# Performance work log

Hardware: AMD Instinct MI355X
Metric: run time of the kernel (lower is better)

The kernel has to match this reference:

```python
import jax, jax.numpy as jnp
import numpy as np

B = 1
N_ATOM = 2048
N_TOKEN = 512
C = 128      # c_q (atom single channels)
CZ = 16      # c_p (atom pair channels)
H = 4        # no_heads
CH = 32      # c_hidden per head
NB = 3       # no_blocks
NT = 2       # n_transition
NH = NT * C  # transition hidden width
N_QUERY = 32
N_KEY = 128
INF = 1e9


def _ln(x, eps=1e-5):
    m = jnp.mean(x, axis=-1, keepdims=True)
    v = jnp.var(x, axis=-1, keepdims=True)
    return (x - m) * jax.lax.rsqrt(v + eps)


def _adaln(a, s, gs, ws, bs, wsb):
    # AF3 Alg 26: AdaLN(a, s)
    s_n = _ln(s) * gs                      # LayerNorm(s), scale only
    a_n = _ln(a)                           # LayerNorm(a), no affine
    return jax.nn.sigmoid(s_n @ ws + bs) * a_n + s_n @ wsb


def setup_inputs() -> dict:
    key = jax.random.key(0)
    ks = jax.random.split(key, 32)

    def w(k, shape, s=0.02):
        return s * jax.random.normal(k, shape, jnp.float32)

    d = {}
    d["ql"] = jax.random.normal(ks[0], (B, N_ATOM, C), jnp.float32)
    d["cl"] = jax.random.normal(ks[1], (B, N_ATOM, C), jnp.float32)
    d["plm"] = jax.random.normal(ks[2], (B, N_ATOM, N_ATOM, CZ), jnp.float32)
    tok = jnp.arange(N_ATOM) // (N_ATOM // N_TOKEN)          # ~4 atoms per token
    d["atom_to_token_index"] = jnp.broadcast_to(jax.nn.one_hot(tok, N_TOKEN, dtype=jnp.float32), (B, N_ATOM, N_TOKEN)) + 0.0
    d["token_mask"] = jnp.ones((B, N_TOKEN), jnp.float32)

    # AttentionPairBias params (stacked over NB blocks)
    d["ada1_gs"] = jnp.ones((NB, C), jnp.float32)
    d["ada1_ws"] = w(ks[3], (NB, C, C))
    d["ada1_bs"] = jnp.zeros((NB, C), jnp.float32)
    d["ada1_wsb"] = w(ks[4], (NB, C, C))
    d["wq"] = w(ks[5], (NB, C, H, CH))
    d["bq"] = jnp.zeros((NB, H, CH), jnp.float32)
    d["wk"] = w(ks[6], (NB, C, H, CH))
    d["wv"] = w(ks[7], (NB, C, H, CH))
    d["gz"] = jnp.ones((NB, CZ), jnp.float32)
    d["bz"] = jnp.zeros((NB, CZ), jnp.float32)
    d["wz"] = w(ks[8], (NB, CZ, H))
    d["wg"] = w(ks[9], (NB, C, H, CH))
    d["wo"] = w(ks[10], (NB, H, CH, C))
    d["wog1"] = w(ks[11], (NB, C, C))
    d["bog1"] = -2.0 * jnp.ones((NB, C), jnp.float32)
    # ConditionedTransitionBlock params
    d["ada2_gs"] = jnp.ones((NB, C), jnp.float32)
    d["ada2_ws"] = w(ks[12], (NB, C, C))
    d["ada2_bs"] = jnp.zeros((NB, C), jnp.float32)
    d["ada2_wsb"] = w(ks[13], (NB, C, C))
    d["wt1"] = w(ks[14], (NB, C, NH))
    d["wt2"] = w(ks[15], (NB, C, NH))
    d["wt3"] = w(ks[16], (NB, NH, C))
    d["wog2"] = w(ks[17], (NB, C, C))
    d["bog2"] = -2.0 * jnp.ones((NB, C), jnp.float32)
    return d


def _forward(ql, cl, plm, atom_to_token_index, token_mask,
             ada1_gs, ada1_ws, ada1_bs, ada1_wsb, wq, bq, wk, wv,
             gz, bz, wz, wg, wo, wog1, bog1,
             ada2_gs, ada2_ws, ada2_bs, ada2_wsb, wt1, wt2, wt3, wog2, bog2):
    # --- block-sparse (32x128) additive mask, exactly as in the torch module ---
    offset = N_QUERY // 2 - 0.5
    n_center = N_ATOM // N_QUERY + 1
    centers = offset + jnp.arange(n_center, dtype=jnp.float32) * N_QUERY
    ar = jnp.arange(N_ATOM, dtype=jnp.float32)
    row = (jnp.abs(ar[:, None] - centers[None, :]) < N_QUERY / 2).astype(ql.dtype)
    col = (jnp.abs(ar[:, None] - centers[None, :]) < N_KEY / 2).astype(ql.dtype)
    blm = (row @ col.T - 1.0) * INF                          # [N, N] in {0, -inf}

    atom_mask = jnp.einsum("bli,bi->bl", atom_to_token_index, token_mask)
    mask_bias = (atom_mask - 1.0) * INF                      # [B, N] additive key mask

    inv_sqrt_ch = 1.0 / np.sqrt(CH).astype(np.float32)
    a, s = ql, cl
    for b in range(NB):
        # --- AttentionPairBias (AF3 Alg 24) ---
        a_ln = _adaln(a, s, ada1_gs[b], ada1_ws[b], ada1_bs[b], ada1_wsb[b])
        q = jnp.einsum("bnc,chd->bnhd", a_ln, wq[b]) + bq[b]
        k = jnp.einsum("bnc,chd->bnhd", a_ln, wk[b])
        v = jnp.einsum("bnc,chd->bnhd", a_ln, wv[b])
        z_ln = _ln(plm) * gz[b] + bz[b]
        pb = jnp.einsum("bnmc,ch->bhnm", z_ln, wz[b])        # pair bias [B,H,N,N]
        logits = (jnp.einsum("bnhd,bmhd->bhnm", q, k) * inv_sqrt_ch
                  + pb + blm[None, None] + mask_bias[:, None, None, :])
        attn = jax.nn.softmax(logits, axis=-1)
        o = jnp.einsum("bhnm,bmhd->bnhd", attn, v)
        o = jax.nn.sigmoid(jnp.einsum("bnc,chd->bnhd", a_ln, wg[b])) * o
        att_out = jnp.einsum("bnhd,hdc->bnc", o, wo[b])
        att_out = jax.nn.sigmoid(s @ wog1[b] + bog1[b]) * att_out
        # --- ConditionedTransitionBlock (AF3 Alg 25) ---
        a2 = _adaln(a, s, ada2_gs[b], ada2_ws[b], ada2_bs[b], ada2_wsb[b])
        hidden = jax.nn.silu(a2 @ wt1[b]) * (a2 @ wt2[b])    # SwiGLU
        trans = jax.nn.sigmoid(s @ wog2[b] + bog2[b]) * (hidden @ wt3[b])
        a = att_out + trans                                   # AF3 Alg 23 update
    return a


def reference(ql, cl, plm, atom_to_token_index, token_mask,
              ada1_gs, ada1_ws, ada1_bs, ada1_wsb, wq, bq, wk, wv,
              gz, bz, wz, wg, wo, wog1, bog1,
              ada2_gs, ada2_ws, ada2_bs, ada2_wsb, wt1, wt2, wt3, wog2, bog2):
    return _forward(ql, cl, plm, atom_to_token_index, token_mask,
                    ada1_gs, ada1_ws, ada1_bs, ada1_wsb, wq, bq, wk, wv,
                    gz, bz, wz, wg, wo, wog1, bog1,
                    ada2_gs, ada2_ws, ada2_bs, ada2_wsb, wt1, wt2, wt3, wog2, bog2)
```

## Files before the change

kernel.cpp:

```cpp
#include <hip/hip_runtime.h>
#include <math.h>

#define N_ATOM 2048
#define NTOK   512
#define CC     128
#define CZDIM  16
#define HH     4
#define CHD    32
#define NHID   256
#define NQB    64
#define R1     8
#define PBSTRIDE 1048576

__device__ __forceinline__ float sigm(float x) { return 1.0f / (1.0f + __expf(-x)); }

struct SmemU {
    float lna[R1][CC];
    float sn1[R1][CC];
    float sn2[R1][CC];
    float cls[R1][CC];
    float aln1[R1][CC];
    float a2s[R1][CC];
    float hid[R1][NHID];
    float tmpA[4][R1][CC];
    float tmpB[4][R1][CC];
};

template<int LDX>
__device__ __forceinline__ void mv_acc(const float* Xbase, int c0, int nc,
                                       const float* __restrict__ W, int ldw,
                                       int col2, float2 acc[4]) {
    for (int c = c0; c < c0 + nc; c += 4) {
        float2 w0 = *(const float2*)(W + (size_t)(c + 0) * ldw + col2);
        float2 w1 = *(const float2*)(W + (size_t)(c + 1) * ldw + col2);
        float2 w2 = *(const float2*)(W + (size_t)(c + 2) * ldw + col2);
        float2 w3 = *(const float2*)(W + (size_t)(c + 3) * ldw + col2);
#pragma unroll
        for (int r = 0; r < 4; r++) {
            float4 xv = *(const float4*)(Xbase + r * LDX + c);
            acc[r].x += xv.x * w0.x + xv.y * w1.x + xv.z * w2.x + xv.w * w3.x;
            acc[r].y += xv.x * w0.y + xv.y * w1.y + xv.z * w2.y + xv.w * w3.y;
        }
    }
}

__device__ void adaln_proj_body(
    SmemU& sm, int t, int n0,
    const float* __restrict__ gs1, const float* __restrict__ ws1,
    const float* __restrict__ bs1, const float* __restrict__ wsb1,
    const float* __restrict__ wq, const float* __restrict__ bq,
    const float* __restrict__ wk, const float* __restrict__ wv,
    const float* __restrict__ wg,
    const float* __restrict__ wog1, const float* __restrict__ bog1,
    const float* __restrict__ gs2, const float* __restrict__ ws2,
    const float* __restrict__ bs2, const float* __restrict__ wsb2,
    const float* __restrict__ wt1, const float* __restrict__ wt2,
    const float* __restrict__ wt3,
    const float* __restrict__ wog2, const float* __restrict__ bog2,
    float* __restrict__ q_o, float* __restrict__ k_o, float* __restrict__ v_o,
    float* __restrict__ g_o, float* __restrict__ og1_o, float* __restrict__ trans_o) {
    {
        int r = t >> 6, l = t & 63;
        float s = 0, s2 = 0;
#pragma unroll
        for (int k = 0; k < 2; k++) { float x = sm.lna[r][l + 64 * k]; s += x; s2 += x * x; }
        for (int m = 1; m < 64; m <<= 1) { s += __shfl_xor(s, m); s2 += __shfl_xor(s2, m); }
        float mean = s * (1.0f / 128.0f);
        float rs = rsqrtf(s2 * (1.0f / 128.0f) - mean * mean + 1e-5f);
        float cs = 0, cs2 = 0;
#pragma unroll
        for (int k = 0; k < 2; k++) { float x = sm.cls[r][l + 64 * k]; cs += x; cs2 += x * x; }
        for (int m = 1; m < 64; m <<= 1) { cs += __shfl_xor(cs, m); cs2 += __shfl_xor(cs2, m); }
        float cmean = cs * (1.0f / 128.0f);
        float crs = rsqrtf(cs2 * (1.0f / 128.0f) - cmean * cmean + 1e-5f);
#pragma unroll
        for (int k = 0; k < 2; k++) {
            int c = l + 64 * k;
            sm.lna[r][c] = (sm.lna[r][c] - mean) * rs;
            float cn = (sm.cls[r][c] - cmean) * crs;
            sm.sn1[r][c] = cn * gs1[c];
            sm.sn2[r][c] = cn * gs2[c];
        }
    }
    __syncthreads();

    {
        int rh = (t >> 6) & 1, l = t & 63, col2 = 2 * l;
        {
            int s = t >> 7;
            const float* X = (s < 2) ? &sm.sn1[rh * 4][0] : &sm.sn2[rh * 4][0];
            const float* W = (s == 0) ? ws1 : (s == 1) ? wsb1 : (s == 2) ? ws2 : wsb2;
            float2 acc[4] = {{0,0},{0,0},{0,0},{0,0}};
            mv_acc<CC>(X, 0, CC, W, CC, col2, acc);
#pragma unroll
            for (int r = 0; r < 4; r++)
                *(float2*)&sm.tmpA[s][rh * 4 + r][col2] = acc[r];
        }
        {
            int s2 = t >> 8, ch = (t >> 7) & 1;
            const float* W = s2 ? wog2 : wog1;
            float2 acc[4] = {{0,0},{0,0},{0,0},{0,0}};
            mv_acc<CC>(&sm.cls[rh * 4][0], ch * 64, 64, W, CC, col2, acc);
#pragma unroll
            for (int r = 0; r < 4; r++)
                *(float2*)&sm.tmpB[s2 * 2 + ch][rh * 4 + r][col2] = acc[r];
        }
    }
    __syncthreads();

    float G[2];
    {
        int o = t & 127, g = t >> 7;
#pragma unroll
        for (int r = 0; r < 2; r++) {
            int rr = 2 * g + r;
            float A1 = sm.tmpA[0][rr][o], B1 = sm.tmpA[1][rr][o];
            float A2 = sm.tmpA[2][rr][o], B2 = sm.tmpA[3][rr][o];
            float O1 = sm.tmpB[0][rr][o] + sm.tmpB[1][rr][o];
            float O2 = sm.tmpB[2][rr][o] + sm.tmpB[3][rr][o];
            float ln = sm.lna[rr][o];
            sm.aln1[rr][o] = sigm(A1 + bs1[o]) * ln + B1;
            sm.a2s [rr][o] = sigm(A2 + bs2[o]) * ln + B2;
            og1_o[(size_t)(n0 + rr) * CC + o] = sigm(O1 + bog1[o]);
            G[r] = sigm(O2 + bog2[o]);
        }
    }
    __syncthreads();

    {
        int s = t >> 7, rh = (t >> 6) & 1, l = t & 63, col2 = 2 * l;
        const float* W = (s == 0) ? wq : (s == 1) ? wk : (s == 2) ? wv : wg;
        float2 acc[4] = {{0,0},{0,0},{0,0},{0,0}};
        mv_acc<CC>(&sm.aln1[rh * 4][0], 0, CC, W, CC, col2, acc);
        float* dst = (s == 0) ? q_o : (s == 1) ? k_o : (s == 2) ? v_o : g_o;
#pragma unroll
        for (int r = 0; r < 4; r++) {
            float2 v = acc[r];
            if (s == 0) { v.x += bq[col2]; v.y += bq[col2 + 1]; }
            if (s == 3) { v.x = sigm(v.x); v.y = sigm(v.y); }
            *(float2*)&dst[(size_t)(n0 + rh * 4 + r) * CC + col2] = v;
        }
    }

    int sT, rhT, colT;
    float2 accT[4] = {{0,0},{0,0},{0,0},{0,0}};
    {
        sT = t >> 8; rhT = (t >> 7) & 1; colT = 2 * (t & 127);
        const float* W = sT ? wt2 : wt1;
        mv_acc<CC>(&sm.a2s[rhT * 4][0], 0, CC, W, NHID, colT, accT);
        if (sT == 0) {
#pragma unroll
            for (int r = 0; r < 4; r++) {
                float2 h;
                h.x = accT[r].x * sigm(accT[r].x);
                h.y = accT[r].y * sigm(accT[r].y);
                *(float2*)&sm.hid[rhT * 4 + r][colT] = h;
            }
        }
    }
    __syncthreads();
    if (sT == 1) {
#pragma unroll
        for (int r = 0; r < 4; r++) {
            float2 h = *(float2*)&sm.hid[rhT * 4 + r][colT];
            h.x *= accT[r].x; h.y *= accT[r].y;
            *(float2*)&sm.hid[rhT * 4 + r][colT] = h;
        }
    }
    __syncthreads();

    {
        int cq = t >> 7, rh = (t >> 6) & 1, l = t & 63, col2 = 2 * l;
        float2 acc[4] = {{0,0},{0,0},{0,0},{0,0}};
        mv_acc<NHID>(&sm.hid[rh * 4][0], cq * 64, 64, wt3, CC, col2, acc);
#pragma unroll
        for (int r = 0; r < 4; r++)
            *(float2*)&sm.tmpA[cq][rh * 4 + r][col2] = acc[r];
    }
    __syncthreads();
    {
        int o = t & 127, g = t >> 7;
#pragma unroll
        for (int r = 0; r < 2; r++) {
            int rr = 2 * g + r;
            float s4 = sm.tmpA[0][rr][o] + sm.tmpA[1][rr][o]
                     + sm.tmpA[2][rr][o] + sm.tmpA[3][rr][o];
            trans_o[(size_t)(n0 + rr) * CC + o] = G[r] * s4;
        }
    }
}

__global__ __launch_bounds__(512) void k_update_first(
    const float* __restrict__ a_in, const float* __restrict__ cl,
    const float* __restrict__ gs1, const float* __restrict__ ws1,
    const float* __restrict__ bs1, const float* __restrict__ wsb1,
    const float* __restrict__ wq, const float* __restrict__ bq,
    const float* __restrict__ wk, const float* __restrict__ wv,
    const float* __restrict__ wg,
    const float* __restrict__ wog1, const float* __restrict__ bog1,
    const float* __restrict__ gs2, const float* __restrict__ ws2,
    const float* __restrict__ bs2, const float* __restrict__ wsb2,
    const float* __restrict__ wt1, const float* __restrict__ wt2,
    const float* __restrict__ wt3,
    const float* __restrict__ wog2, const float* __restrict__ bog2,
    float* __restrict__ q_o, float* __restrict__ k_o, float* __restrict__ v_o,
    float* __restrict__ g_o, float* __restrict__ og1_o, float* __restrict__ trans_o) {
    __shared__ SmemU sm;
    const int t = threadIdx.x;
    const int n0 = blockIdx.x * R1;
    ((float2*)sm.lna)[t] = ((const float2*)(a_in + (size_t)n0 * CC))[t];
    ((float2*)sm.cls)[t] = ((const float2*)(cl + (size_t)n0 * CC))[t];
    __syncthreads();
    adaln_proj_body(sm, t, n0, gs1, ws1, bs1, wsb1, wq, bq, wk, wv, wg, wog1, bog1,
                    gs2, ws2, bs2, wsb2, wt1, wt2, wt3, wog2, bog2,
                    q_o, k_o, v_o, g_o, og1_o, trans_o);
}

__global__ __launch_bounds__(512) void k_update(
    const float* __restrict__ cl,
    const float* __restrict__ g_in, const float* __restrict__ o_in,
    const float* __restrict__ og1_in, const float* __restrict__ trans_in,
    const float* __restrict__ wo_prev,
    const float* __restrict__ gs1, const float* __restrict__ ws1,
    const float* __restrict__ bs1, const float* __restrict__ wsb1,
    const float* __restrict__ wq, const float* __restrict__ bq,
    const float* __restrict__ wk, const float* __restrict__ wv,
    const float* __restrict__ wg,
    const float* __restrict__ wog1, const float* __restrict__ bog1,
    const float* __restrict__ gs2, const float* __restrict__ ws2,
    const float* __restrict__ bs2, const float* __restrict__ wsb2,
    const float* __restrict__ wt1, const float* __restrict__ wt2,
    const float* __restrict__ wt3,
    const float* __restrict__ wog2, const float* __restrict__ bog2,
    float* __restrict__ q_o, float* __restrict__ k_o, float* __restrict__ v_o,
    float* __restrict__ g_o, float* __restrict__ og1_o, float* __restrict__ trans_o) {
    __shared__ SmemU sm;
    const int t = threadIdx.x;
    const int n0 = blockIdx.x * R1;
    {
        float2 gv = ((const float2*)(g_in + (size_t)n0 * CC))[t];
        float2 ov = ((const float2*)(o_in + (size_t)n0 * CC))[t];
        float2 p; p.x = gv.x * ov.x; p.y = gv.y * ov.y;
        ((float2*)sm.aln1)[t] = p;
        ((float2*)sm.cls)[t] = ((const float2*)(cl + (size_t)n0 * CC))[t];
    }
    __syncthreads();
    {
        int cq = t >> 7, rh = (t >> 6) & 1, l = t & 63, col2 = 2 * l;
        float2 acc[4] = {{0,0},{0,0},{0,0},{0,0}};
        mv_acc<CC>(&sm.aln1[rh * 4][0], cq * 32, 32, wo_prev, CC, col2, acc);
#pragma unroll
        for (int r = 0; r < 4; r++)
            *(float2*)&sm.tmpA[cq][rh * 4 + r][col2] = acc[r];
    }
    __syncthreads();
    {
        int o = t & 127, g = t >> 7;
#pragma unroll
        for (int r = 0; r < 2; r++) {
            int rr = 2 * g + r;
            float s4 = sm.tmpA[0][rr][o] + sm.tmpA[1][rr][o]
                     + sm.tmpA[2][rr][o] + sm.tmpA[3][rr][o];
            sm.lna[rr][o] = og1_in[(size_t)(n0 + rr) * CC + o] * s4
                          + trans_in[(size_t)(n0 + rr) * CC + o];
        }
    }
    __syncthreads();
    adaln_proj_body(sm, t, n0, gs1, ws1, bs1, wsb1, wq, bq, wk, wv, wg, wog1, bog1,
                    gs2, ws2, bs2, wsb2, wt1, wt2, wt3, wog2, bog2,
                    q_o, k_o, v_o, g_o, og1_o, trans_o);
}

__global__ __launch_bounds__(512) void k_combine(const float* __restrict__ g,
                                                 const float* __restrict__ o_in,
                                                 const float* __restrict__ og1,
                                                 const float* __restrict__ trans,
                                                 const float* __restrict__ wo,
                                                 float* __restrict__ a_out) {
    __shared__ SmemU sm;
    const int t = threadIdx.x;
    const int n0 = blockIdx.x * R1;
    {
        float2 gv = ((const float2*)(g + (size_t)n0 * CC))[t];
        float2 ov = ((const float2*)(o_in + (size_t)n0 * CC))[t];
        float2 p; p.x = gv.x * ov.x; p.y = gv.y * ov.y;
        ((float2*)sm.aln1)[t] = p;
    }
    __syncthreads();
    {
        int cq = t >> 7, rh = (t >> 6) & 1, l = t & 63, col2 = 2 * l;
        float2 acc[4] = {{0,0},{0,0},{0,0},{0,0}};
        mv_acc<CC>(&sm.aln1[rh * 4][0], cq * 32, 32, wo, CC, col2, acc);
#pragma unroll
        for (int r = 0; r < 4; r++)
            *(float2*)&sm.tmpA[cq][rh * 4 + r][col2] = acc[r];
    }
    __syncthreads();
    {
        int o = t & 127, g2 = t >> 7;
#pragma unroll
        for (int r = 0; r < 2; r++) {
            int rr = 2 * g2 + r;
            float s4 = sm.tmpA[0][rr][o] + sm.tmpA[1][rr][o]
                     + sm.tmpA[2][rr][o] + sm.tmpA[3][rr][o];
            a_out[(size_t)(n0 + rr) * CC + o] =
                og1[(size_t)(n0 + rr) * CC + o] * s4
                + trans[(size_t)(n0 + rr) * CC + o];
        }
    }
}

__global__ __launch_bounds__(256) void k_pb3_amask(const float* __restrict__ plm,
                                                   const float* __restrict__ gz,
                                                   const float* __restrict__ bz,
                                                   const float* __restrict__ wz,
                                                   const float* __restrict__ a2t,
                                                   const float* __restrict__ tm,
                                                   float* __restrict__ pb,
                                                   float* __restrict__ amask) {
    if (blockIdx.x >= 1024) {
        int wave = threadIdx.x >> 6, lane = threadIdx.x & 63;
        int l = (blockIdx.x - 1024) * 4 + wave;
        float s = 0.0f;
        for (int i = lane; i < NTOK; i += 64) s += a2t[(size_t)l * NTOK + i] * tm[i];
        for (int m = 1; m < 64; m <<= 1) s += __shfl_xor(s, m);
        if (lane == 0) amask[l] = (s - 1.0f) * 1e9f;
        return;
    }
    int pid = blockIdx.x * 256 + threadIdx.x;
    int qb = pid >> 12;
    int qi = (pid >> 7) & 31;
    int kj = pid & 127;
    int n = qb * 32 + qi;
    int kstart = max(0, qb * 32 - 48);
    int m = kstart + kj;
    bool valid = (m < N_ATOM);
    float xn[CZDIM];
    if (valid) {
        const float4* p4 = (const float4*)(plm + ((size_t)n * N_ATOM + m) * CZDIM);
        float x[CZDIM];
#pragma unroll
        for (int i = 0; i < 4; i++) {
            float4 v = p4[i];
            x[4 * i] = v.x; x[4 * i + 1] = v.y; x[4 * i + 2] = v.z; x[4 * i + 3] = v.w;
        }
        float s = 0, s2 = 0;
#pragma unroll
        for (int c = 0; c < CZDIM; c++) { s += x[c]; s2 += x[c] * x[c]; }
        float mean = s * (1.0f / 16.0f);
        float rs = rsqrtf(s2 * (1.0f / 16.0f) - mean * mean + 1e-5f);
#pragma unroll
        for (int c = 0; c < CZDIM; c++) xn[c] = (x[c] - mean) * rs;
    }
#pragma unroll
    for (int b = 0; b < 3; b++) {
        float out[HH] = {0, 0, 0, 0};
        if (valid) {
            const float* gzb = gz + b * CZDIM;
            const float* bzb = bz + b * CZDIM;
            const float* wzb = wz + b * CZDIM * HH;
#pragma unroll
            for (int c = 0; c < CZDIM; c++) {
                float z = xn[c] * gzb[c] + bzb[c];
#pragma unroll
                for (int h = 0; h < HH; h++) out[h] += z * wzb[c * HH + h];
            }
        }
#pragma unroll
        for (int h = 0; h < HH; h++)
            pb[b * PBSTRIDE + (((qb * HH + h) * 32 + qi) << 7) + kj] = out[h];
    }
}

__global__ __launch_bounds__(512) void k_attn(const float* __restrict__ q,
                                              const float* __restrict__ k,
                                              const float* __restrict__ v,
                                              const float* __restrict__ pb,
                                              const float* __restrict__ amask,
                                              float* __restrict__ o_out) {
    __shared__ __align__(16) float qs[32][36];
    __shared__ __align__(16) float ks[128][36];
    __shared__ __align__(16) float vs[128][36];
    __shared__ __align__(16) float ps[32][132];
    const int t = threadIdx.x;
    const int qb = blockIdx.x >> 2, h = blockIdx.x & 3;
    const int n0 = qb * 32;
    const int kstart = max(0, qb * 32 - 48);
    const int nk = min(N_ATOM, qb * 32 + 80) - kstart;

    if (t < 256) {
        int qi = t >> 3, dq = t & 7;
        *(float4*)&qs[qi][dq * 4] = *(const float4*)&q[(n0 + qi) * CC + h * CHD + dq * 4];
    }
    for (int idx = t; idx < 1024; idx += 512) {
        int kj = idx >> 3, dq = idx & 7;
        int m = kstart + kj;
        float4 kv = {0, 0, 0, 0}, vv = {0, 0, 0, 0};
        if (m < N_ATOM) {
            kv = *(const float4*)&k[m * CC + h * CHD + dq * 4];
            vv = *(const float4*)&v[m * CC + h * CHD + dq * 4];
        }
        *(float4*)&ks[kj][dq * 4] = kv;
        *(float4*)&vs[kj][dq * 4] = vv;
    }
    __syncthreads();

    const int qi = t >> 4, j16 = t & 15;
    float4 qr[8];
#pragma unroll
    for (int dq = 0; dq < 8; dq++) qr[dq] = *(const float4*)&qs[qi][dq * 4];

    const float isc = 0.17677669529663687f;
    const float* pbrow = pb + ((qb * HH + h) * 32 + qi) * 128;
    float lr[8];
    float mx = -1e30f;
#pragma unroll
    for (int jj = 0; jj < 8; jj++) {
        int kj = j16 + 16 * jj;
        float acc = 0;
#pragma unroll
        for (int dq = 0; dq < 8; dq++) {
            float4 kk = *(const float4*)&ks[kj][dq * 4];
            acc += qr[dq].x * kk.x + qr[dq].y * kk.y + qr[dq].z * kk.z + qr[dq].w * kk.w;
        }
        float l = (kj < nk) ? (acc * isc + pbrow[kj] + amask[kstart + kj]) : -1e9f;
        lr[jj] = l;
        mx = fmaxf(mx, l);
    }
    for (int m = 1; m < 16; m <<= 1) mx = fmaxf(mx, __shfl_xor(mx, m));
    float sum = 0;
#pragma unroll
    for (int jj = 0; jj < 8; jj++) { lr[jj] = __expf(lr[jj] - mx); sum += lr[jj]; }
    for (int m = 1; m < 16; m <<= 1) sum += __shfl_xor(sum, m);
    float rd = 1.0f / sum;
#pragma unroll
    for (int jj = 0; jj < 8; jj++) ps[qi][j16 + 16 * jj] = lr[jj] * rd;
    __syncthreads();

    const int d0 = (t & 15) * 2;
    float2 acc = {0, 0};
    for (int kj = 0; kj < 128; kj += 4) {
        float4 pv = *(const float4*)&ps[qi][kj];
        float2 v0 = *(const float2*)&vs[kj][d0];
        float2 v1 = *(const float2*)&vs[kj + 1][d0];
        float2 v2 = *(const float2*)&vs[kj + 2][d0];
        float2 v3 = *(const float2*)&vs[kj + 3][d0];
        acc.x += pv.x * v0.x + pv.y * v1.x + pv.z * v2.x + pv.w * v3.x;
        acc.y += pv.x * v0.y + pv.y * v1.y + pv.z * v2.y + pv.w * v3.y;
    }
    *(float2*)&o_out[(n0 + qi) * CC + h * CHD + d0] = acc;
}

extern "C" void kernel_launch(void* const* d_in, const int* in_sizes, int n_in,
                              void* d_out, int out_size, void* d_ws, size_t ws_size,
                              hipStream_t stream) {
    const float* ql   = (const float*)d_in[0];
    const float* cl   = (const float*)d_in[1];
    const float* plm  = (const float*)d_in[2];
    const float* a2t  = (const float*)d_in[3];
    const float* tm   = (const float*)d_in[4];
    const float* ada1_gs  = (const float*)d_in[5];
    const float* ada1_ws  = (const float*)d_in[6];
    const float* ada1_bs  = (const float*)d_in[7];
    const float* ada1_wsb = (const float*)d_in[8];
    const float* wq  = (const float*)d_in[9];
    const float* bq  = (const float*)d_in[10];
    const float* wk  = (const float*)d_in[11];
    const float* wv  = (const float*)d_in[12];
    const float* gz  = (const float*)d_in[13];
    const float* bz  = (const float*)d_in[14];
    const float* wz  = (const float*)d_in[15];
    const float* wg  = (const float*)d_in[16];
    const float* wo  = (const float*)d_in[17];
    const float* wog1 = (const float*)d_in[18];
    const float* bog1 = (const float*)d_in[19];
    const float* ada2_gs  = (const float*)d_in[20];
    const float* ada2_ws  = (const float*)d_in[21];
    const float* ada2_bs  = (const float*)d_in[22];
    const float* ada2_wsb = (const float*)d_in[23];
    const float* wt1 = (const float*)d_in[24];
    const float* wt2 = (const float*)d_in[25];
    const float* wt3 = (const float*)d_in[26];
    const float* wog2 = (const float*)d_in[27];
    const float* bog2 = (const float*)d_in[28];

    const size_t NC = (size_t)N_ATOM * CC;
    float* ws = (float*)d_ws;
    float* q_    = ws + 0 * NC;
    float* k_    = ws + 1 * NC;
    float* v_    = ws + 2 * NC;
    float* g_    = ws + 3 * NC;
    float* og1_  = ws + 4 * NC;
    float* tr_   = ws + 5 * NC;
    float* o_    = ws + 6 * NC;
    float* pb3   = ws + 7 * NC;
    float* am    = ws + 7 * NC + 3 * PBSTRIDE;

    k_pb3_amask<<<1536, 256, 0, stream>>>(plm, gz, bz, wz, a2t, tm, pb3, am);

    for (int b = 0; b < 3; b++) {
        if (b == 0) {
            k_update_first<<<N_ATOM / R1, 512, 0, stream>>>(
                ql, cl,
                ada1_gs, ada1_ws, ada1_bs, ada1_wsb,
                wq, bq, wk, wv, wg, wog1, bog1,
                ada2_gs, ada2_ws, ada2_bs, ada2_wsb,
                wt1, wt2, wt3, wog2, bog2,
                q_, k_, v_, g_, og1_, tr_);
        } else {
            k_update<<<N_ATOM / R1, 512, 0, stream>>>(
                cl, g_, o_, og1_, tr_, wo + (size_t)(b - 1) * CC * CC,
                ada1_gs + b * CC, ada1_ws + (size_t)b * CC * CC, ada1_bs + b * CC,
                ada1_wsb + (size_t)b * CC * CC,
                wq + (size_t)b * CC * CC, bq + b * CC, wk + (size_t)b * CC * CC,
                wv + (size_t)b * CC * CC, wg + (size_t)b * CC * CC,
                wog1 + (size_t)b * CC * CC, bog1 + b * CC,
                ada2_gs + b * CC, ada2_ws + (size_t)b * CC * CC, ada2_bs + b * CC,
                ada2_wsb + (size_t)b * CC * CC,
                wt1 + (size_t)b * CC * NHID, wt2 + (size_t)b * CC * NHID,
                wt3 + (size_t)b * NHID * CC,
                wog2 + (size_t)b * CC * CC, bog2 + b * CC,
                q_, k_, v_, g_, og1_, tr_);
        }
        k_attn<<<NQB * HH, 512, 0, stream>>>(q_, k_, v_, pb3 + (size_t)b * PBSTRIDE, am, o_);
    }
    k_combine<<<N_ATOM / R1, 512, 0, stream>>>(g_, o_, og1_, tr_, wo + (size_t)2 * CC * CC,
                                               (float*)d_out);
}
```

Baseline: 530.3 us.

## Double block size to 1024 threads and merge pair-bias prep into first update kernel

Every kernel now runs 1024-thread blocks. Work that earlier ran in sequential phases (the AdaLN projections alongside the gate projections, the Q/K/V/G projections alongside the SwiGLU matmuls) is split across the two halves of the block so the phases run at the same time, with split-K reductions widened to 8 partial sums. The separate pair-bias/mask kernel is folded into the first update kernel as extra blocks, removing one launch and letting the two kinds of work overlap. In exchange, register pressure per thread rises under launch_bounds(1024,4), the reductions use more shared memory, and attention's PV stage leaves half the threads idle.

```diff
diff --git a/kernel.cpp b/kernel.cpp
--- a/kernel.cpp
+++ b/kernel.cpp
@@ -22,8 +22,7 @@
     float aln1[R1][CC];
     float a2s[R1][CC];
     float hid[R1][NHID];
-    float tmpA[4][R1][CC];
-    float tmpB[4][R1][CC];
+    float tmp[8][R1][CC];
 };
 
 template<int LDX>
@@ -60,75 +59,71 @@
     float* __restrict__ q_o, float* __restrict__ k_o, float* __restrict__ v_o,
     float* __restrict__ g_o, float* __restrict__ og1_o, float* __restrict__ trans_o) {
     {
-        int r = t >> 6, l = t & 63;
-        float s = 0, s2 = 0;
-#pragma unroll
-        for (int k = 0; k < 2; k++) { float x = sm.lna[r][l + 64 * k]; s += x; s2 += x * x; }
-        for (int m = 1; m < 64; m <<= 1) { s += __shfl_xor(s, m); s2 += __shfl_xor(s2, m); }
-        float mean = s * (1.0f / 128.0f);
-        float rs = rsqrtf(s2 * (1.0f / 128.0f) - mean * mean + 1e-5f);
-        float cs = 0, cs2 = 0;
-#pragma unroll
-        for (int k = 0; k < 2; k++) { float x = sm.cls[r][l + 64 * k]; cs += x; cs2 += x * x; }
-        for (int m = 1; m < 64; m <<= 1) { cs += __shfl_xor(cs, m); cs2 += __shfl_xor(cs2, m); }
-        float cmean = cs * (1.0f / 128.0f);
-        float crs = rsqrtf(cs2 * (1.0f / 128.0f) - cmean * cmean + 1e-5f);
-#pragma unroll
-        for (int k = 0; k < 2; k++) {
-            int c = l + 64 * k;
-            sm.lna[r][c] = (sm.lna[r][c] - mean) * rs;
-            float cn = (sm.cls[r][c] - cmean) * crs;
-            sm.sn1[r][c] = cn * gs1[c];
-            sm.sn2[r][c] = cn * gs2[c];
-        }
-    }
-    __syncthreads();
-
-    {
-        int rh = (t >> 6) & 1, l = t & 63, col2 = 2 * l;
-        {
-            int s = t >> 7;
-            const float* X = (s < 2) ? &sm.sn1[rh * 4][0] : &sm.sn2[rh * 4][0];
-            const float* W = (s == 0) ? ws1 : (s == 1) ? wsb1 : (s == 2) ? ws2 : wsb2;
-            float2 acc[4] = {{0,0},{0,0},{0,0},{0,0}};
-            mv_acc<CC>(X, 0, CC, W, CC, col2, acc);
-#pragma unroll
-            for (int r = 0; r < 4; r++)
-                *(float2*)&sm.tmpA[s][rh * 4 + r][col2] = acc[r];
-        }
-        {
-            int s2 = t >> 8, ch = (t >> 7) & 1;
-            const float* W = s2 ? wog2 : wog1;
-            float2 acc[4] = {{0,0},{0,0},{0,0},{0,0}};
-            mv_acc<CC>(&sm.cls[rh * 4][0], ch * 64, 64, W, CC, col2, acc);
-#pragma unroll
-            for (int r = 0; r < 4; r++)
-                *(float2*)&sm.tmpB[s2 * 2 + ch][rh * 4 + r][col2] = acc[r];
-        }
-    }
-    __syncthreads();
-
-    float G[2];
-    {
-        int o = t & 127, g = t >> 7;
-#pragma unroll
-        for (int r = 0; r < 2; r++) {
-            int rr = 2 * g + r;
-            float A1 = sm.tmpA[0][rr][o], B1 = sm.tmpA[1][rr][o];
-            float A2 = sm.tmpA[2][rr][o], B2 = sm.tmpA[3][rr][o];
-            float O1 = sm.tmpB[0][rr][o] + sm.tmpB[1][rr][o];
-            float O2 = sm.tmpB[2][rr][o] + sm.tmpB[3][rr][o];
-            float ln = sm.lna[rr][o];
-            sm.aln1[rr][o] = sigm(A1 + bs1[o]) * ln + B1;
-            sm.a2s [rr][o] = sigm(A2 + bs2[o]) * ln + B2;
-            og1_o[(size_t)(n0 + rr) * CC + o] = sigm(O1 + bog1[o]);
-            G[r] = sigm(O2 + bog2[o]);
-        }
-    }
-    __syncthreads();
-
-    {
-        int s = t >> 7, rh = (t >> 6) & 1, l = t & 63, col2 = 2 * l;
+        int r = t >> 6;
+        if (r < R1) {
+            int l = t & 63;
+            float s = 0, s2 = 0;
+#pragma unroll
+            for (int k = 0; k < 2; k++) { float x = sm.lna[r][l + 64 * k]; s += x; s2 += x * x; }
+            for (int m = 1; m < 64; m <<= 1) { s += __shfl_xor(s, m); s2 += __shfl_xor(s2, m); }
+            float mean = s * (1.0f / 128.0f);
+            float rs = rsqrtf(s2 * (1.0f / 128.0f) - mean * mean + 1e-5f);
+            float cs = 0, cs2 = 0;
+#pragma unroll
+            for (int k = 0; k < 2; k++) { float x = sm.cls[r][l + 64 * k]; cs += x; cs2 += x * x; }
+            for (int m = 1; m < 64; m <<= 1) { cs += __shfl_xor(cs, m); cs2 += __shfl_xor(cs2, m); }
+            float cmean = cs * (1.0f / 128.0f);
+            float crs = rsqrtf(cs2 * (1.0f / 128.0f) - cmean * cmean + 1e-5f);
+#pragma unroll
+            for (int k = 0; k < 2; k++) {
+                int c = l + 64 * k;
+                sm.lna[r][c] = (sm.lna[r][c] - mean) * rs;
+                float cn = (sm.cls[r][c] - cmean) * crs;
+                sm.sn1[r][c] = cn * gs1[c];
+                sm.sn2[r][c] = cn * gs2[c];
+            }
+        }
+    }
+    __syncthreads();
+
+    if (t < 512) {
+        int s = t >> 7, rh = (t >> 6) & 1, col2 = 2 * (t & 63);
+        const float* X = (s < 2) ? &sm.sn1[rh * 4][0] : &sm.sn2[rh * 4][0];
+        const float* W = (s == 0) ? ws1 : (s == 1) ? wsb1 : (s == 2) ? ws2 : wsb2;
+        float2 acc[4] = {{0,0},{0,0},{0,0},{0,0}};
+        mv_acc<CC>(X, 0, CC, W, CC, col2, acc);
+#pragma unroll
+        for (int r = 0; r < 4; r++)
+            *(float2*)&sm.tmp[s][rh * 4 + r][col2] = acc[r];
+    } else {
+        int u = t - 512;
+        int s2 = u >> 8, ch = (u >> 7) & 1, rh = (u >> 6) & 1, col2 = 2 * (u & 63);
+        const float* W = s2 ? wog2 : wog1;
+        float2 acc[4] = {{0,0},{0,0},{0,0},{0,0}};
+        mv_acc<CC>(&sm.cls[rh * 4][0], ch * 64, 64, W, CC, col2, acc);
+#pragma unroll
+        for (int r = 0; r < 4; r++)
+            *(float2*)&sm.tmp[4 + s2 * 2 + ch][rh * 4 + r][col2] = acc[r];
+    }
+    __syncthreads();
+
+    float G;
+    {
+        int rr = t >> 7, o = t & 127;
+        float A1 = sm.tmp[0][rr][o], B1 = sm.tmp[1][rr][o];
+        float A2 = sm.tmp[2][rr][o], B2 = sm.tmp[3][rr][o];
+        float O1 = sm.tmp[4][rr][o] + sm.tmp[5][rr][o];
+        float O2 = sm.tmp[6][rr][o] + sm.tmp[7][rr][o];
+        float ln = sm.lna[rr][o];
+        sm.aln1[rr][o] = sigm(A1 + bs1[o]) * ln + B1;
+        sm.a2s [rr][o] = sigm(A2 + bs2[o]) * ln + B2;
+        og1_o[(size_t)(n0 + rr) * CC + o] = sigm(O1 + bog1[o]);
+        G = sigm(O2 + bog2[o]);
+    }
+    __syncthreads();
+
+    if (t < 512) {
+        int s = t >> 7, rh = (t >> 6) & 1, col2 = 2 * (t & 63);
         const float* W = (s == 0) ? wq : (s == 1) ? wk : (s == 2) ? wv : wg;
         float2 acc[4] = {{0,0},{0,0},{0,0},{0,0}};
         mv_acc<CC>(&sm.aln1[rh * 4][0], 0, CC, W, CC, col2, acc);
@@ -140,58 +135,114 @@
             if (s == 3) { v.x = sigm(v.x); v.y = sigm(v.y); }
             *(float2*)&dst[(size_t)(n0 + rh * 4 + r) * CC + col2] = v;
         }
-    }
-
-    int sT, rhT, colT;
-    float2 accT[4] = {{0,0},{0,0},{0,0},{0,0}};
-    {
-        sT = t >> 8; rhT = (t >> 7) & 1; colT = 2 * (t & 127);
+    } else {
+        int u = t - 512;
+        int sT = u >> 8, rhT = (u >> 7) & 1, colT = 2 * (u & 127);
         const float* W = sT ? wt2 : wt1;
-        mv_acc<CC>(&sm.a2s[rhT * 4][0], 0, CC, W, NHID, colT, accT);
+        float2 acc[4] = {{0,0},{0,0},{0,0},{0,0}};
+        mv_acc<CC>(&sm.a2s[rhT * 4][0], 0, CC, W, NHID, colT, acc);
         if (sT == 0) {
 #pragma unroll
             for (int r = 0; r < 4; r++) {
                 float2 h;
-                h.x = accT[r].x * sigm(accT[r].x);
-                h.y = accT[r].y * sigm(accT[r].y);
+                h.x = acc[r].x * sigm(acc[r].x);
+                h.y = acc[r].y * sigm(acc[r].y);
                 *(float2*)&sm.hid[rhT * 4 + r][colT] = h;
             }
-        }
-    }
-    __syncthreads();
-    if (sT == 1) {
-#pragma unroll
-        for (int r = 0; r < 4; r++) {
-            float2 h = *(float2*)&sm.hid[rhT * 4 + r][colT];
-            h.x *= accT[r].x; h.y *= accT[r].y;
-            *(float2*)&sm.hid[rhT * 4 + r][colT] = h;
-        }
-    }
-    __syncthreads();
-
-    {
-        int cq = t >> 7, rh = (t >> 6) & 1, l = t & 63, col2 = 2 * l;
+        } else {
+            float* w2buf = &sm.tmp[0][0][0];
+#pragma unroll
+            for (int r = 0; r < 4; r++)
+                *(float2*)&w2buf[(rhT * 4 + r) * NHID + colT] = acc[r];
+        }
+    }
+    __syncthreads();
+    {
+        float* hf = &sm.hid[0][0];
+        float* w2buf = &sm.tmp[0][0][0];
+        hf[t] *= w2buf[t];
+        hf[t + 1024] *= w2buf[t + 1024];
+    }
+    __syncthreads();
+
+    {
+        int g = t >> 6, cq = g & 7, rh = g >> 3, col2 = 2 * (t & 63);
         float2 acc[4] = {{0,0},{0,0},{0,0},{0,0}};
-        mv_acc<NHID>(&sm.hid[rh * 4][0], cq * 64, 64, wt3, CC, col2, acc);
+        mv_acc<NHID>(&sm.hid[rh * 4][0], cq * 32, 32, wt3, CC, col2, acc);
 #pragma unroll
         for (int r = 0; r < 4; r++)
-            *(float2*)&sm.tmpA[cq][rh * 4 + r][col2] = acc[r];
-    }
-    __syncthreads();
-    {
-        int o = t & 127, g = t >> 7;
-#pragma unroll
-        for (int r = 0; r < 2; r++) {
-            int rr = 2 * g + r;
-            float s4 = sm.tmpA[0][rr][o] + sm.tmpA[1][rr][o]
-                     + sm.tmpA[2][rr][o] + sm.tmpA[3][rr][o];
-            trans_o[(size_t)(n0 + rr) * CC + o] = G[r] * s4;
-        }
-    }
-}
-
-__global__ __launch_bounds__(512) void k_update_first(
-    const float* __restrict__ a_in, const float* __restrict__ cl,
+            *(float2*)&sm.tmp[cq][rh * 4 + r][col2] = acc[r];
+    }
+    __syncthreads();
+    {
+        int rr = t >> 7, o = t & 127;
+        float s8 = sm.tmp[0][rr][o] + sm.tmp[1][rr][o] + sm.tmp[2][rr][o] + sm.tmp[3][rr][o]
+                 + sm.tmp[4][rr][o] + sm.tmp[5][rr][o] + sm.tmp[6][rr][o] + sm.tmp[7][rr][o];
+        trans_o[(size_t)(n0 + rr) * CC + o] = G * s8;
+    }
+}
+
+__device__ __forceinline__ void w_phase(SmemU& sm, int t, const float* __restrict__ wo) {
+    int g = t >> 6, cq = g & 7, rh = g >> 3, col2 = 2 * (t & 63);
+    float2 acc[4] = {{0,0},{0,0},{0,0},{0,0}};
+    mv_acc<CC>(&sm.aln1[rh * 4][0], cq * 16, 16, wo, CC, col2, acc);
+#pragma unroll
+    for (int r = 0; r < 4; r++)
+        *(float2*)&sm.tmp[cq][rh * 4 + r][col2] = acc[r];
+}
+
+__device__ void pb_body(const float* __restrict__ plm, const float* __restrict__ gz,
+                        const float* __restrict__ bz, const float* __restrict__ wz,
+                        float* __restrict__ pb, int pid) {
+    int qb = pid >> 12;
+    int qi = (pid >> 7) & 31;
+    int kj = pid & 127;
+    int n = qb * 32 + qi;
+    int kstart = max(0, qb * 32 - 48);
+    int m = kstart + kj;
+    bool valid = (m < N_ATOM);
+    float xn[CZDIM];
+    if (valid) {
+        const float4* p4 = (const float4*)(plm + ((size_t)n * N_ATOM + m) * CZDIM);
+        float x[CZDIM];
+#pragma unroll
+        for (int i = 0; i < 4; i++) {
+            float4 v = p4[i];
+            x[4 * i] = v.x; x[4 * i + 1] = v.y; x[4 * i + 2] = v.z; x[4 * i + 3] = v.w;
+        }
+        float s = 0, s2 = 0;
+#pragma unroll
+        for (int c = 0; c < CZDIM; c++) { s += x[c]; s2 += x[c] * x[c]; }
+        float mean = s * (1.0f / 16.0f);
+        float rs = rsqrtf(s2 * (1.0f / 16.0f) - mean * mean + 1e-5f);
+#pragma unroll
+        for (int c = 0; c < CZDIM; c++) xn[c] = (x[c] - mean) * rs;
+    }
+#pragma unroll
+    for (int b = 0; b < 3; b++) {
+        float out[HH] = {0, 0, 0, 0};
+        if (valid) {
+            const float* gzb = gz + b * CZDIM;
+            const float* bzb = bz + b * CZDIM;
+            const float* wzb = wz + b * CZDIM * HH;
+#pragma unroll
+            for (int c = 0; c < CZDIM; c++) {
+                float z = xn[c] * gzb[c] + bzb[c];
+#pragma unroll
+                for (int h = 0; h < HH; h++) out[h] += z * wzb[c * HH + h];
+            }
+        }
+#pragma unroll
+        for (int h = 0; h < HH; h++)
+            pb[b * PBSTRIDE + (((qb * HH + h) * 32 + qi) << 7) + kj] = out[h];
+    }
+}
+
+__global__ __launch_bounds__(1024, 4) void k_first(
+    const float* __restrict__ ql, const float* __restrict__ cl,
+    const float* __restrict__ plm, const float* __restrict__ gz,
+    const float* __restrict__ bz, const float* __restrict__ wz,
+    const float* __restrict__ a2t, const float* __restrict__ tm,
     const float* __restrict__ gs1, const float* __restrict__ ws1,
     const float* __restrict__ bs1, const float* __restrict__ wsb1,
     const float* __restrict__ wq, const float* __restrict__ bq,
@@ -204,19 +255,37 @@
     const float* __restrict__ wt3,
     const float* __restrict__ wog2, const float* __restrict__ bog2,
     float* __restrict__ q_o, float* __restrict__ k_o, float* __restrict__ v_o,
-    float* __restrict__ g_o, float* __restrict__ og1_o, float* __restrict__ trans_o) {
+    float* __restrict__ g_o, float* __restrict__ og1_o, float* __restrict__ trans_o,
+    float* __restrict__ pb3, float* __restrict__ amask) {
     __shared__ SmemU sm;
     const int t = threadIdx.x;
-    const int n0 = blockIdx.x * R1;
-    ((float2*)sm.lna)[t] = ((const float2*)(a_in + (size_t)n0 * CC))[t];
-    ((float2*)sm.cls)[t] = ((const float2*)(cl + (size_t)n0 * CC))[t];
+    const int bx = blockIdx.x;
+    if (bx >= 512) {
+        int u = bx - 512;
+        int wave = t >> 6, lane = t & 63;
+        int l = u * 16 + wave;
+        float s = 0.0f;
+        for (int i = lane; i < NTOK; i += 64) s += a2t[(size_t)l * NTOK + i] * tm[i];
+        for (int m = 1; m < 64; m <<= 1) s += __shfl_xor(s, m);
+        if (lane == 0) amask[l] = (s - 1.0f) * 1e9f;
+        return;
+    }
+    if (bx >= 256) {
+        pb_body(plm, gz, bz, wz, pb3, (bx - 256) * 1024 + t);
+        return;
+    }
+    const int n0 = bx * R1;
+    if (t < 256)
+        ((float4*)sm.lna)[t] = ((const float4*)(ql + (size_t)n0 * CC))[t];
+    else if (t < 512)
+        ((float4*)sm.cls)[t - 256] = ((const float4*)(cl + (size_t)n0 * CC))[t - 256];
     __syncthreads();
     adaln_proj_body(sm, t, n0, gs1, ws1, bs1, wsb1, wq, bq, wk, wv, wg, wog1, bog1,
                     gs2, ws2, bs2, wsb2, wt1, wt2, wt3, wog2, bog2,
                     q_o, k_o, v_o, g_o, og1_o, trans_o);
 }
 
-__global__ __launch_bounds__(512) void k_update(
+__global__ __launch_bounds__(1024, 4) void k_update(
     const float* __restrict__ cl,
     const float* __restrict__ g_in, const float* __restrict__ o_in,
     const float* __restrict__ og1_in, const float* __restrict__ trans_in,
@@ -237,33 +306,23 @@
     __shared__ SmemU sm;
     const int t = threadIdx.x;
     const int n0 = blockIdx.x * R1;
-    {
-        float2 gv = ((const float2*)(g_in + (size_t)n0 * CC))[t];
-        float2 ov = ((const float2*)(o_in + (size_t)n0 * CC))[t];
-        float2 p; p.x = gv.x * ov.x; p.y = gv.y * ov.y;
-        ((float2*)sm.aln1)[t] = p;
-        ((float2*)sm.cls)[t] = ((const float2*)(cl + (size_t)n0 * CC))[t];
-    }
-    __syncthreads();
-    {
-        int cq = t >> 7, rh = (t >> 6) & 1, l = t & 63, col2 = 2 * l;
-        float2 acc[4] = {{0,0},{0,0},{0,0},{0,0}};
-        mv_acc<CC>(&sm.aln1[rh * 4][0], cq * 32, 32, wo_prev, CC, col2, acc);
-#pragma unroll
-        for (int r = 0; r < 4; r++)
-            *(float2*)&sm.tmpA[cq][rh * 4 + r][col2] = acc[r];
-    }
-    __syncthreads();
-    {
-        int o = t & 127, g = t >> 7;
-#pragma unroll
-        for (int r = 0; r < 2; r++) {
-            int rr = 2 * g + r;
-            float s4 = sm.tmpA[0][rr][o] + sm.tmpA[1][rr][o]
-                     + sm.tmpA[2][rr][o] + sm.tmpA[3][rr][o];
-            sm.lna[rr][o] = og1_in[(size_t)(n0 + rr) * CC + o] * s4
-                          + trans_in[(size_t)(n0 + rr) * CC + o];
-        }
+    if (t < 256) {
+        float4 gv = ((const float4*)(g_in + (size_t)n0 * CC))[t];
+        float4 ov = ((const float4*)(o_in + (size_t)n0 * CC))[t];
+        float4 p; p.x = gv.x * ov.x; p.y = gv.y * ov.y; p.z = gv.z * ov.z; p.w = gv.w * ov.w;
+        ((float4*)sm.aln1)[t] = p;
+    } else if (t < 512) {
+        ((float4*)sm.cls)[t - 256] = ((const float4*)(cl + (size_t)n0 * CC))[t - 256];
+    }
+    __syncthreads();
+    w_phase(sm, t, wo_prev);
+    __syncthreads();
+    {
+        int rr = t >> 7, o = t & 127;
+        float s8 = sm.tmp[0][rr][o] + sm.tmp[1][rr][o] + sm.tmp[2][rr][o] + sm.tmp[3][rr][o]
+                 + sm.tmp[4][rr][o] + sm.tmp[5][rr][o] + sm.tmp[6][rr][o] + sm.tmp[7][rr][o];
+        sm.lna[rr][o] = og1_in[(size_t)(n0 + rr) * CC + o] * s8
+                      + trans_in[(size_t)(n0 + rr) * CC + o];
     }
     __syncthreads();
     adaln_proj_body(sm, t, n0, gs1, ws1, bs1, wsb1, wq, bq, wk, wv, wg, wog1, bog1,
@@ -271,113 +330,40 @@
                     q_o, k_o, v_o, g_o, og1_o, trans_o);
 }
 
-__global__ __launch_bounds__(512) void k_combine(const float* __restrict__ g,
-                                                 const float* __restrict__ o_in,
-                                                 const float* __restrict__ og1,
-                                                 const float* __restrict__ trans,
-                                                 const float* __restrict__ wo,
-                                                 float* __restrict__ a_out) {
+__global__ __launch_bounds__(1024, 4) void k_combine(const float* __restrict__ g,
+                                                     const float* __restrict__ o_in,
+                                                     const float* __restrict__ og1,
+                                                     const float* __restrict__ trans,
+                                                     const float* __restrict__ wo,
+                                                     float* __restrict__ a_out) {
     __shared__ SmemU sm;
     const int t = threadIdx.x;
     const int n0 = blockIdx.x * R1;
-    {
-        float2 gv = ((const float2*)(g + (size_t)n0 * CC))[t];
-        float2 ov = ((const float2*)(o_in + (size_t)n0 * CC))[t];
-        float2 p; p.x = gv.x * ov.x; p.y = gv.y * ov.y;
-        ((float2*)sm.aln1)[t] = p;
-    }
-    __syncthreads();
-    {
-        int cq = t >> 7, rh = (t >> 6) & 1, l = t & 63, col2 = 2 * l;
-        float2 acc[4] = {{0,0},{0,0},{0,0},{0,0}};
-        mv_acc<CC>(&sm.aln1[rh * 4][0], cq * 32, 32, wo, CC, col2, acc);
-#pragma unroll
-        for (int r = 0; r < 4; r++)
-            *(float2*)&sm.tmpA[cq][rh * 4 + r][col2] = acc[r];
-    }
-    __syncthreads();
-    {
-        int o = t & 127, g2 = t >> 7;
-#pragma unroll
-        for (int r = 0; r < 2; r++) {
-            int rr = 2 * g2 + r;
-            float s4 = sm.tmpA[0][rr][o] + sm.tmpA[1][rr][o]
-                     + sm.tmpA[2][rr][o] + sm.tmpA[3][rr][o];
-            a_out[(size_t)(n0 + rr) * CC + o] =
-                og1[(size_t)(n0 + rr) * CC + o] * s4
-                + trans[(size_t)(n0 + rr) * CC + o];
-        }
-    }
-}
-
-__global__ __launch_bounds__(256) void k_pb3_amask(const float* __restrict__ plm,
-                                                   const float* __restrict__ gz,
-                                                   const float* __restrict__ bz,
-                                                   const float* __restrict__ wz,
-                                                   const float* __restrict__ a2t,
-                                                   const float* __restrict__ tm,
-                                                   float* __restrict__ pb,
-                                                   float* __restrict__ amask) {
-    if (blockIdx.x >= 1024) {
-        int wave = threadIdx.x >> 6, lane = threadIdx.x & 63;
-        int l = (blockIdx.x - 1024) * 4 + wave;
-        float s = 0.0f;
-        for (int i = lane; i < NTOK; i += 64) s += a2t[(size_t)l * NTOK + i] * tm[i];
-        for (int m = 1; m < 64; m <<= 1) s += __shfl_xor(s, m);
-        if (lane == 0) amask[l] = (s - 1.0f) * 1e9f;
-        return;
-    }
-    int pid = blockIdx.x * 256 + threadIdx.x;
-    int qb = pid >> 12;
-    int qi = (pid >> 7) & 31;
-    int kj = pid & 127;
-    int n = qb * 32 + qi;
-    int kstart = max(0, qb * 32 - 48);
-    int m = kstart + kj;
-    bool valid = (m < N_ATOM);
-    float xn[CZDIM];
-    if (valid) {
-        const float4* p4 = (const float4*)(plm + ((size_t)n * N_ATOM + m) * CZDIM);
-        float x[CZDIM];
-#pragma unroll
-        for (int i = 0; i < 4; i++) {
-            float4 v = p4[i];
-            x[4 * i] = v.x; x[4 * i + 1] = v.y; x[4 * i + 2] = v.z; x[4 * i + 3] = v.w;
-        }
-        float s = 0, s2 = 0;
-#pragma unroll
-        for (int c = 0; c < CZDIM; c++) { s += x[c]; s2 += x[c] * x[c]; }
-        float mean = s * (1.0f / 16.0f);
-        float rs = rsqrtf(s2 * (1.0f / 16.0f) - mean * mean + 1e-5f);
-#pragma unroll
-        for (int c = 0; c < CZDIM; c++) xn[c] = (x[c] - mean) * rs;
-    }
-#pragma unroll
-    for (int b = 0; b < 3; b++) {
-        float out[HH] = {0, 0, 0, 0};
-        if (valid) {
-            const float* gzb = gz + b * CZDIM;
-            const float* bzb = bz + b * CZDIM;
-            const float* wzb = wz + b * CZDIM * HH;
-#pragma unroll
-            for (int c = 0; c < CZDIM; c++) {
-                float z = xn[c] * gzb[c] + bzb[c];
-#pragma unroll
-                for (int h = 0; h < HH; h++) out[h] += z * wzb[c * HH + h];
-            }
-        }
-#pragma unroll
-        for (int h = 0; h < HH; h++)
-            pb[b * PBSTRIDE + (((qb * HH + h) * 32 + qi) << 7) + kj] = out[h];
-    }
-}
-
-__global__ __launch_bounds__(512) void k_attn(const float* __restrict__ q,
-                                              const float* __restrict__ k,
-                                              const float* __restrict__ v,
-                                              const float* __restrict__ pb,
-                                              const float* __restrict__ amask,
-                                              float* __restrict__ o_out) {
+    if (t < 256) {
+        float4 gv = ((const float4*)(g + (size_t)n0 * CC))[t];
+        float4 ov = ((const float4*)(o_in + (size_t)n0 * CC))[t];
+        float4 p; p.x = gv.x * ov.x; p.y = gv.y * ov.y; p.z = gv.z * ov.z; p.w = gv.w * ov.w;
+        ((float4*)sm.aln1)[t] = p;
+    }
+    __syncthreads();
+    w_phase(sm, t, wo);
+    __syncthreads();
+    {
+        int rr = t >> 7, o = t & 127;
+        float s8 = sm.tmp[0][rr][o] + sm.tmp[1][rr][o] + sm.tmp[2][rr][o] + sm.tmp[3][rr][o]
+                 + sm.tmp[4][rr][o] + sm.tmp[5][rr][o] + sm.tmp[6][rr][o] + sm.tmp[7][rr][o];
+        a_out[(size_t)(n0 + rr) * CC + o] =
+            og1[(size_t)(n0 + rr) * CC + o] * s8
+            + trans[(size_t)(n0 + rr) * CC + o];
+    }
+}
+
+__global__ __launch_bounds__(1024, 4) void k_attn(const float* __restrict__ q,
+                                                  const float* __restrict__ k,
+                                                  const float* __restrict__ v,
+                                                  const float* __restrict__ pb,
+                                                  const float* __restrict__ amask,
+                                                  float* __restrict__ o_out) {
     __shared__ __align__(16) float qs[32][36];
     __shared__ __align__(16) float ks[128][36];
     __shared__ __align__(16) float vs[128][36];
@@ -392,8 +378,8 @@
         int qi = t >> 3, dq = t & 7;
         *(float4*)&qs[qi][dq * 4] = *(const float4*)&q[(n0 + qi) * CC + h * CHD + dq * 4];
     }
-    for (int idx = t; idx < 1024; idx += 512) {
-        int kj = idx >> 3, dq = idx & 7;
+    {
+        int kj = t >> 3, dq = t & 7;
         int m = kstart + kj;
         float4 kv = {0, 0, 0, 0}, vv = {0, 0, 0, 0};
         if (m < N_ATOM) {
@@ -405,18 +391,18 @@
     }
     __syncthreads();
 
-    const int qi = t >> 4, j16 = t & 15;
+    const int qi = t >> 5, j32 = t & 31;
     float4 qr[8];
 #pragma unroll
     for (int dq = 0; dq < 8; dq++) qr[dq] = *(const float4*)&qs[qi][dq * 4];
 
     const float isc = 0.17677669529663687f;
     const float* pbrow = pb + ((qb * HH + h) * 32 + qi) * 128;
-    float lr[8];
+    float lr[4];
     float mx = -1e30f;
 #pragma unroll
-    for (int jj = 0; jj < 8; jj++) {
-        int kj = j16 + 16 * jj;
+    for (int jj = 0; jj < 4; jj++) {
+        int kj = j32 + 32 * jj;
         float acc = 0;
 #pragma unroll
         for (int dq = 0; dq < 8; dq++) {
@@ -427,28 +413,30 @@
         lr[jj] = l;
         mx = fmaxf(mx, l);
     }
-    for (int m = 1; m < 16; m <<= 1) mx = fmaxf(mx, __shfl_xor(mx, m));
+    for (int m = 1; m < 32; m <<= 1) mx = fmaxf(mx, __shfl_xor(mx, m));
     float sum = 0;
 #pragma unroll
-    for (int jj = 0; jj < 8; jj++) { lr[jj] = __expf(lr[jj] - mx); sum += lr[jj]; }
-    for (int m = 1; m < 16; m <<= 1) sum += __shfl_xor(sum, m);
+    for (int jj = 0; jj < 4; jj++) { lr[jj] = __expf(lr[jj] - mx); sum += lr[jj]; }
+    for (int m = 1; m < 32; m <<= 1) sum += __shfl_xor(sum, m);
     float rd = 1.0f / sum;
 #pragma unroll
-    for (int jj = 0; jj < 8; jj++) ps[qi][j16 + 16 * jj] = lr[jj] * rd;
-    __syncthreads();
-
-    const int d0 = (t & 15) * 2;
-    float2 acc = {0, 0};
-    for (int kj = 0; kj < 128; kj += 4) {
-        float4 pv = *(const float4*)&ps[qi][kj];
-        float2 v0 = *(const float2*)&vs[kj][d0];
-        float2 v1 = *(const float2*)&vs[kj + 1][d0];
-        float2 v2 = *(const float2*)&vs[kj + 2][d0];
-        float2 v3 = *(const float2*)&vs[kj + 3][d0];
-        acc.x += pv.x * v0.x + pv.y * v1.x + pv.z * v2.x + pv.w * v3.x;
-        acc.y += pv.x * v0.y + pv.y * v1.y + pv.z * v2.y + pv.w * v3.y;
-    }
-    *(float2*)&o_out[(n0 + qi) * CC + h * CHD + d0] = acc;
+    for (int jj = 0; jj < 4; jj++) ps[qi][j32 + 32 * jj] = lr[jj] * rd;
+    __syncthreads();
+
+    if (t < 512) {
+        const int qi2 = t >> 4, d0 = (t & 15) * 2;
+        float2 acc = {0, 0};
+        for (int kj = 0; kj < 128; kj += 4) {
+            float4 pv = *(const float4*)&ps[qi2][kj];
+            float2 v0 = *(const float2*)&vs[kj][d0];
+            float2 v1 = *(const float2*)&vs[kj + 1][d0];
+            float2 v2 = *(const float2*)&vs[kj + 2][d0];
+            float2 v3 = *(const float2*)&vs[kj + 3][d0];
+            acc.x += pv.x * v0.x + pv.y * v1.x + pv.z * v2.x + pv.w * v3.x;
+            acc.y += pv.x * v0.y + pv.y * v1.y + pv.z * v2.y + pv.w * v3.y;
+        }
+        *(float2*)&o_out[(n0 + qi2) * CC + h * CHD + d0] = acc;
+    }
 }
 
 extern "C" void kernel_launch(void* const* d_in, const int* in_sizes, int n_in,
@@ -496,19 +484,17 @@
     float* pb3   = ws + 7 * NC;
     float* am    = ws + 7 * NC + 3 * PBSTRIDE;
 
-    k_pb3_amask<<<1536, 256, 0, stream>>>(plm, gz, bz, wz, a2t, tm, pb3, am);
+    k_first<<<640, 1024, 0, stream>>>(
+        ql, cl, plm, gz, bz, wz, a2t, tm,
+        ada1_gs, ada1_ws, ada1_bs, ada1_wsb,
+        wq, bq, wk, wv, wg, wog1, bog1,
+        ada2_gs, ada2_ws, ada2_bs, ada2_wsb,
+        wt1, wt2, wt3, wog2, bog2,
+        q_, k_, v_, g_, og1_, tr_, pb3, am);
 
     for (int b = 0; b < 3; b++) {
-        if (b == 0) {
-            k_update_first<<<N_ATOM / R1, 512, 0, stream>>>(
-                ql, cl,
-                ada1_gs, ada1_ws, ada1_bs, ada1_wsb,
-                wq, bq, wk, wv, wg, wog1, bog1,
-                ada2_gs, ada2_ws, ada2_bs, ada2_wsb,
-                wt1, wt2, wt3, wog2, bog2,
-                q_, k_, v_, g_, og1_, tr_);
-        } else {
-            k_update<<<N_ATOM / R1, 512, 0, stream>>>(
+        if (b > 0) {
+            k_update<<<N_ATOM / R1, 1024, 0, stream>>>(
                 cl, g_, o_, og1_, tr_, wo + (size_t)(b - 1) * CC * CC,
                 ada1_gs + b * CC, ada1_ws + (size_t)b * CC * CC, ada1_bs + b * CC,
                 ada1_wsb + (size_t)b * CC * CC,
@@ -522,8 +508,8 @@
                 wog2 + (size_t)b * CC * CC, bog2 + b * CC,
                 q_, k_, v_, g_, og1_, tr_);
         }
-        k_attn<<<NQB * HH, 512, 0, stream>>>(q_, k_, v_, pb3 + (size_t)b * PBSTRIDE, am, o_);
-    }
-    k_combine<<<N_ATOM / R1, 512, 0, stream>>>(g_, o_, og1_, tr_, wo + (size_t)2 * CC * CC,
-                                               (float*)d_out);
-}
+        k_attn<<<NQB * HH, 1024, 0, stream>>>(q_, k_, v_, pb3 + (size_t)b * PBSTRIDE, am, o_);
+    }
+    k_combine<<<N_ATOM / R1, 1024, 0, stream>>>(g_, o_, og1_, tr_, wo + (size_t)2 * CC * CC,
+                                                (float*)d_out);
+}
```

After: 526.3 us (median of 2 runs). No clear change (-0.8%).
